# Kernel optimization log

Measured on AMD Instinct MI355X. Metric: run time of the kernel, lower is better.

Reference implementation:

```python
import jax, jax.numpy as jnp
import numpy as np

N_TEAMS = 100000
N_EDGES = 1600000
BATCH = 16384
DIM = 64
SLOPE = 0.01  # torch leaky_relu default


def setup_inputs() -> dict:
    key = jax.random.key(0)
    ks = jax.random.split(key, 12)
    return {
        "edge_index": jax.random.randint(ks[0], (2, N_EDGES), 0, N_TEAMS, dtype=jnp.int32),
        "edge_weight": jax.random.uniform(ks[1], (N_EDGES,), dtype=jnp.float32),
        "home": jax.random.randint(ks[2], (BATCH,), 0, N_TEAMS, dtype=jnp.int32),
        "away": jax.random.randint(ks[3], (BATCH,), 0, N_TEAMS, dtype=jnp.int32),
        "emb": jax.random.normal(ks[4], (N_TEAMS, DIM), dtype=jnp.float32),
        "W0": jax.random.normal(ks[5], (DIM, DIM), dtype=jnp.float32) * 0.1,
        "b0": jnp.zeros((DIM,), jnp.float32),
        "W1": jax.random.normal(ks[6], (DIM, DIM), dtype=jnp.float32) * 0.1,
        "b1": jnp.zeros((DIM,), jnp.float32),
        "W2": jax.random.normal(ks[7], (DIM, DIM), dtype=jnp.float32) * 0.1,
        "b2": jnp.zeros((DIM,), jnp.float32),
        "lin1_W": jax.random.normal(ks[8], (2 * DIM, 6), dtype=jnp.float32) * 0.1,
        "lin1_b": jnp.zeros((6,), jnp.float32),
        "lin3_W": jax.random.normal(ks[9], (6, 3), dtype=jnp.float32) * 0.1,
        "lin3_b": jnp.zeros((3,), jnp.float32),
    }


def gcn_conv(x, W, b, src, dst, w, n):
    """PyG GCNConv: add self-loops, symmetric edge-weight norm, gather-scale-scatter."""
    xw = x @ W  # [N, D_out]
    loop = jnp.arange(n, dtype=src.dtype)
    src2 = jnp.concatenate([src, loop])
    dst2 = jnp.concatenate([dst, loop])
    w2 = jnp.concatenate([w, jnp.ones((n,), x.dtype)])
    deg = jax.ops.segment_sum(w2, dst2, num_segments=n)
    dinv = jnp.where(deg > 0, jax.lax.rsqrt(jnp.maximum(deg, 1e-12)), 0.0)
    norm = dinv[src2] * w2 * dinv[dst2]  # [E+N]
    msgs = norm[:, None] * xw[src2]  # irregular gather, [E+N, D_out]
    return jax.ops.segment_sum(msgs, dst2, num_segments=n) + b


def reference(edge_index, edge_weight, home, away, emb, W0, b0, W1, b1, W2, b2,
              lin1_W, lin1_b, lin3_W, lin3_b):
    src, dst = edge_index[0], edge_index[1]
    n = emb.shape[0]
    x = emb  # embedding lookup of arange(n_teams) == full table
    x = jax.nn.leaky_relu(gcn_conv(x, W0, b0, src, dst, edge_weight, n), SLOPE)
    x = jax.nn.leaky_relu(gcn_conv(x, W1, b1, src, dst, edge_weight, n), SLOPE)
    x = jax.nn.leaky_relu(gcn_conv(x, W2, b2, src, dst, edge_weight, n), SLOPE)
    h = jnp.concatenate([x[home], x[away]], axis=-1)  # [B, 2*D]
    h = jax.nn.leaky_relu(h @ lin1_W + lin1_b, SLOPE)
    h = jax.nn.leaky_relu(h @ lin3_W + lin3_b, SLOPE)
    out = jax.nn.log_softmax(h, axis=0)  # original uses LogSoftmax(dim=0)
    return out.reshape(-1, 3)
```

## Files before the change

### kernel.cpp

```cpp
#include <hip/hip_runtime.h>
#include <hip/hip_fp8.h>
#include <math.h>

#define N_TEAMS 100000
#define N_EDGES 1600000
#define BATCH   16384
#define DIM     64
#define SLOPE   0.01f
#define NPAD    100352
#define BSHIFT  6
#define BROWS   64
#define NB      1563
#define SLOTS   8
#define SCAP    256

__device__ __forceinline__ float leaky(float v) { return v > 0.f ? v : SLOPE * v; }

__device__ __forceinline__ float bf2f(unsigned short u) {
    return __uint_as_float(((unsigned)u) << 16);
}
__device__ __forceinline__ unsigned short f2bf(float f) {
    unsigned b = __float_as_uint(f);
    unsigned r = b + 0x7FFFu + ((b >> 16) & 1u);
    return (unsigned short)(r >> 16);
}
__device__ __forceinline__ float f82f(unsigned char u) {
    __hip_fp8_e4m3 v; v.__x = (__hip_fp8_storage_t)u;
    return (float)v;
}
__device__ __forceinline__ unsigned char f2f8(float f) {
    __hip_fp8_e4m3 v(f);
    return (unsigned char)v.__x;
}
__device__ __forceinline__ float pw2f(unsigned p) {
    return __uint_as_float((p & 0xFFFE0000u) >> 1);
}


__global__ void k_zerob(int* __restrict__ bcnt) {
    int i = blockIdx.x * blockDim.x + threadIdx.x;
    if (i < NB * SLOTS) bcnt[i * 16] = 0;
}

__global__ void k_part(const int* __restrict__ src, const int* __restrict__ dst,
                       const float* __restrict__ w, int* __restrict__ bcnt,
                       unsigned long long* __restrict__ pbuf, int E) {
    int e = blockIdx.x * blockDim.x + threadIdx.x;
    if (e >= E) return;
    int slot = blockIdx.x & (SLOTS - 1);
    int s = __builtin_nontemporal_load(src + e);
    int d = __builtin_nontemporal_load(dst + e);
    float wv = __builtin_nontemporal_load(w + e);
    unsigned pk = (((unsigned)f2bf(wv) & 0x7FFFu) << 17) | (unsigned)s;
    int cell = (d >> BSHIFT) * SLOTS + slot;
    int p = atomicAdd(&bcnt[cell * 16], 1);
    pbuf[(size_t)cell * SCAP + p] = (((unsigned long long)d) << 32) | pk;
}

__global__ __launch_bounds__(256) void k_bcnt(const int* __restrict__ bcnt,
                                              const unsigned long long* __restrict__ pbuf,
                                              int* __restrict__ cnt) {
    __shared__ int h[BROWS];
    int b = blockIdx.x, tid = threadIdx.x;
    if (tid < BROWS) h[tid] = 0;
    __syncthreads();
    for (int slot = 0; slot < SLOTS; slot++) {
        int cell = b * SLOTS + slot;
        int n = bcnt[cell * 16];
        const unsigned long long* pb = pbuf + (size_t)cell * SCAP;
        for (int i = tid; i < n; i += 256) {
            int d = (int)(pb[i] >> 32);
            atomicAdd(&h[d & (BROWS - 1)], 1);
        }
    }
    __syncthreads();
    int row = b * BROWS + tid;
    if (tid < BROWS && row < NPAD) cnt[row] = h[tid];
}

__global__ __launch_bounds__(256) void k_scatter(const int* __restrict__ bcnt,
                                                 const unsigned long long* __restrict__ pbuf,
                                                 const int* __restrict__ row_start,
                                                 unsigned* __restrict__ edges) {
    __shared__ int fl[BROWS];
    int b = blockIdx.x, tid = threadIdx.x;
    if (tid < BROWS) fl[tid] = 0;
    __syncthreads();
    for (int slot = 0; slot < SLOTS; slot++) {
        int cell = b * SLOTS + slot;
        int n = bcnt[cell * 16];
        const unsigned long long* pb = pbuf + (size_t)cell * SCAP;
        for (int i = tid; i < n; i += 256) {
            unsigned long long rec = pb[i];
            int d = (int)(rec >> 32);
            int p = atomicAdd(&fl[d & (BROWS - 1)], 1);
            edges[row_start[d] + p] = (unsigned)rec;
        }
    }
}


__global__ __launch_bounds__(1024) void k_scan1(const int* __restrict__ cnt,
                                                int* __restrict__ excl,
                                                int* __restrict__ partial, int n) {
    __shared__ int s[1024];
    int tid = threadIdx.x;
    int i = blockIdx.x * 1024 + tid;
    int v = (i < n) ? cnt[i] : 0;
    s[tid] = v;
    __syncthreads();
    for (int off = 1; off < 1024; off <<= 1) {
        int t = (tid >= off) ? s[tid - off] : 0;
        __syncthreads();
        s[tid] += t;
        __syncthreads();
    }
    excl[i] = s[tid] - v;
    if (tid == 1023) partial[blockIdx.x] = s[1023];
}

__global__ __launch_bounds__(128) void k_scan2(int* __restrict__ partial, int nb) {
    __shared__ int s[128];
    int tid = threadIdx.x;
    int v = (tid < nb) ? partial[tid] : 0;
    s[tid] = v;
    __syncthreads();
    for (int off = 1; off < 128; off <<= 1) {
        int t = (tid >= off) ? s[tid - off] : 0;
        __syncthreads();
        s[tid] += t;
        __syncthreads();
    }
    if (tid < nb) partial[tid] = s[tid] - v;
}

__global__ __launch_bounds__(1024) void k_scan3(int* __restrict__ row_start,
                                                const int* __restrict__ partial) {
    int i = blockIdx.x * 1024 + threadIdx.x;
    row_start[i] += partial[blockIdx.x];
}


__global__ void k_dinv(const int* __restrict__ row_start,
                       const unsigned* __restrict__ edges,
                       float* __restrict__ dinv, int n) {
    int r = blockIdx.x * blockDim.x + threadIdx.x;
    if (r >= n) return;
    int beg = row_start[r], end = row_start[r + 1];
    float s = 1.0f;
    for (int j = beg; j < end; j++) s += pw2f(edges[j]);
    dinv[r] = rsqrtf(fmaxf(s, 1e-12f));
}


__global__ void k_cvt(const float* __restrict__ emb, unsigned short* __restrict__ y,
                      int n4) {
    int i = blockIdx.x * blockDim.x + threadIdx.x;
    if (i >= n4) return;
    float4 v = ((const float4*)emb)[i];
    ushort4 o;
    o.x = f2bf(v.x); o.y = f2bf(v.y); o.z = f2bf(v.z); o.w = f2bf(v.w);
    ((ushort4*)y)[i] = o;
}


__global__ __launch_bounds__(256) void k_gemm(
    const unsigned short* __restrict__ y, const float* __restrict__ W,
    const float* __restrict__ dinv, unsigned char* __restrict__ t8, int n) {
    __shared__ float Ws[64 * 64];
    __shared__ float xs[16 * 64];
    int tid = threadIdx.x;
    const float4* Wv = (const float4*)W;
    float4* Wsv = (float4*)Ws;
#pragma unroll
    for (int i = 0; i < 4; i++) Wsv[tid + i * 256] = Wv[tid + i * 256];
    int row0 = blockIdx.x * 16;
    {
        int idx = tid * 4;
        int r = idx >> 6, cc = idx & 63;
        ushort4 v = *(const ushort4*)(y + (((size_t)(row0 + r)) << 6) + cc);
        xs[idx + 0] = bf2f(v.x); xs[idx + 1] = bf2f(v.y);
        xs[idx + 2] = bf2f(v.z); xs[idx + 3] = bf2f(v.w);
    }
    __syncthreads();
    int c = tid & 63, rr = tid >> 6;
    float acc[4] = {0.f, 0.f, 0.f, 0.f};
#pragma unroll
    for (int k = 0; k < 64; k++) {
        float wv = Ws[k * 64 + c];
#pragma unroll
        for (int i = 0; i < 4; i++) acc[i] = fmaf(xs[(4 * i + rr) * 64 + k], wv, acc[i]);
    }
#pragma unroll
    for (int i = 0; i < 4; i++) {
        int r = row0 + 4 * i + rr;
        t8[(((size_t)r) << 6) + c] = f2f8(dinv[r] * acc[i]);
    }
}


__global__ __launch_bounds__(256) void k_agg(
    const unsigned char* __restrict__ t8, const int* __restrict__ row_start,
    const unsigned* __restrict__ edges, const float* __restrict__ dinv,
    const float* __restrict__ b, unsigned short* __restrict__ y, int n) {
    int tid = threadIdx.x;
    int lane = tid & 63;
    int row = blockIdx.x * 4 + (tid >> 6);
    if (row >= n) return;
    float bl = b[lane];
    int beg = row_start[row];
    int c = row_start[row + 1] - beg;
    float di = dinv[row];
    float acc = f82f(t8[((unsigned)row << 6) + lane]);
    const unsigned* ep = edges + beg;
    int j = 0;
    int chunks = c >> 3;
    if (chunks > 0) {
        unsigned ev[8];
#pragma unroll
        for (int k = 0; k < 8; k++) ev[k] = __builtin_nontemporal_load(ep + k);
        for (int t = 1; t <= chunks; t++) {
            float nv[8], xv[8];
#pragma unroll
            for (int k = 0; k < 8; k++) {
                int s = (int)(ev[k] & 0x1FFFFu);
                nv[k] = pw2f(ev[k]);
                xv[k] = f82f(t8[((unsigned)s << 6) + lane]);
            }
            if (t < chunks) {
                const unsigned* np = ep + (size_t)t * 8;
#pragma unroll
                for (int k = 0; k < 8; k++) ev[k] = __builtin_nontemporal_load(np + k);
            }
#pragma unroll
            for (int k = 0; k < 8; k++) acc = fmaf(nv[k], xv[k], acc);
        }
        j = chunks * 8;
    }
    if (j + 4 <= c) {
        unsigned e0 = __builtin_nontemporal_load(ep + j + 0);
        unsigned e1 = __builtin_nontemporal_load(ep + j + 1);
        unsigned e2 = __builtin_nontemporal_load(ep + j + 2);
        unsigned e3 = __builtin_nontemporal_load(ep + j + 3);
        float x0 = f82f(t8[((e0 & 0x1FFFFu) << 6) + lane]);
        float x1 = f82f(t8[((e1 & 0x1FFFFu) << 6) + lane]);
        float x2 = f82f(t8[((e2 & 0x1FFFFu) << 6) + lane]);
        float x3 = f82f(t8[((e3 & 0x1FFFFu) << 6) + lane]);
        acc = fmaf(pw2f(e0), x0, acc);
        acc = fmaf(pw2f(e1), x1, acc);
        acc = fmaf(pw2f(e2), x2, acc);
        acc = fmaf(pw2f(e3), x3, acc);
        j += 4;
    }
    for (; j < c; j++) {
        unsigned e0 = __builtin_nontemporal_load(ep + j);
        acc = fmaf(pw2f(e0), f82f(t8[((e0 & 0x1FFFFu) << 6) + lane]), acc);
    }
    y[((unsigned)row << 6) + lane] = f2bf(leaky(fmaf(di, acc, bl)));
}


__global__ __launch_bounds__(256) void k_head(
    const unsigned short* __restrict__ xb, const int* __restrict__ home,
    const int* __restrict__ away, const float* __restrict__ W1,
    const float* __restrict__ b1, const float* __restrict__ W3,
    const float* __restrict__ b3, float* __restrict__ z2, int B) {
    __shared__ float W1s[128 * 6];
    __shared__ float b1s[6], W3s[18], b3s[3];
    int tid = threadIdx.x;
    for (int i = tid; i < 768; i += 256) W1s[i] = W1[i];
    if (tid < 6) b1s[tid] = b1[tid];
    if (tid < 18) W3s[tid] = W3[tid];
    if (tid < 3) b3s[tid] = b3[tid];
    __syncthreads();
    int i = blockIdx.x * 256 + tid;
    if (i >= B) return;
    float z1[6];
#pragma unroll
    for (int j = 0; j < 6; j++) z1[j] = b1s[j];
    const uint4* rows[2];
    rows[0] = (const uint4*)(xb + (size_t)home[i] * 64);
    rows[1] = (const uint4*)(xb + (size_t)away[i] * 64);
#pragma unroll
    for (int h = 0; h < 2; h++) {
        const uint4* r = rows[h];
        int base = h * 64;
#pragma unroll
        for (int k = 0; k < 8; k++) {
            uint4 v = r[k];
            unsigned uu[4] = {v.x, v.y, v.z, v.w};
#pragma unroll
            for (int t = 0; t < 4; t++) {
                float fx = bf2f((unsigned short)(uu[t] & 0xFFFF));
                float fy = bf2f((unsigned short)(uu[t] >> 16));
                int d = base + k * 8 + t * 2;
#pragma unroll
                for (int j = 0; j < 6; j++) {
                    z1[j] = fmaf(fx, W1s[d * 6 + j], z1[j]);
                    z1[j] = fmaf(fy, W1s[(d + 1) * 6 + j], z1[j]);
                }
            }
        }
    }
#pragma unroll
    for (int j = 0; j < 6; j++) z1[j] = leaky(z1[j]);
#pragma unroll
    for (int c = 0; c < 3; c++) {
        float s = b3s[c];
#pragma unroll
        for (int j = 0; j < 6; j++) s = fmaf(z1[j], W3s[j * 3 + c], s);
        z2[(size_t)i * 3 + c] = leaky(s);
    }
}


__global__ __launch_bounds__(1024) void k_stats(const float* __restrict__ z2,
                                                float* __restrict__ stats, int B) {
    __shared__ float red[3][1024];
    int tid = threadIdx.x;
    float m[3] = {-1e30f, -1e30f, -1e30f};
    for (int i = tid; i < B; i += 1024) {
        m[0] = fmaxf(m[0], z2[3 * i + 0]);
        m[1] = fmaxf(m[1], z2[3 * i + 1]);
        m[2] = fmaxf(m[2], z2[3 * i + 2]);
    }
    for (int c = 0; c < 3; c++) red[c][tid] = m[c];
    __syncthreads();
    for (int s = 512; s > 0; s >>= 1) {
        if (tid < s)
            for (int c = 0; c < 3; c++) red[c][tid] = fmaxf(red[c][tid], red[c][tid + s]);
        __syncthreads();
    }
    float M[3];
    for (int c = 0; c < 3; c++) M[c] = red[c][0];
    __syncthreads();
    float sum[3] = {0.f, 0.f, 0.f};
    for (int i = tid; i < B; i += 1024) {
        sum[0] += expf(z2[3 * i + 0] - M[0]);
        sum[1] += expf(z2[3 * i + 1] - M[1]);
        sum[2] += expf(z2[3 * i + 2] - M[2]);
    }
    for (int c = 0; c < 3; c++) red[c][tid] = sum[c];
    __syncthreads();
    for (int s = 512; s > 0; s >>= 1) {
        if (tid < s)
            for (int c = 0; c < 3; c++) red[c][tid] += red[c][tid + s];
        __syncthreads();
    }
    if (tid == 0)
        for (int c = 0; c < 3; c++) { stats[c] = M[c]; stats[3 + c] = logf(red[c][0]); }
}

__global__ void k_final(const float* __restrict__ z2, const float* __restrict__ stats,
                        float* __restrict__ out, int n) {
    int i = blockIdx.x * blockDim.x + threadIdx.x;
    if (i < n) {
        int c = i % 3;
        out[i] = z2[i] - stats[c] - stats[3 + c];
    }
}


extern "C" void kernel_launch(void* const* d_in, const int* in_sizes, int n_in,
                              void* d_out, int out_size, void* d_ws, size_t ws_size,
                              hipStream_t stream) {
    const int*   edge_index = (const int*)d_in[0];
    const int*   src  = edge_index;
    const int*   dst  = edge_index + N_EDGES;
    const float* ew   = (const float*)d_in[1];
    const int*   home = (const int*)d_in[2];
    const int*   away = (const int*)d_in[3];
    const float* emb  = (const float*)d_in[4];
    const float* W0 = (const float*)d_in[5];  const float* b0 = (const float*)d_in[6];
    const float* W1 = (const float*)d_in[7];  const float* b1 = (const float*)d_in[8];
    const float* W2 = (const float*)d_in[9];  const float* b2 = (const float*)d_in[10];
    const float* l1W = (const float*)d_in[11]; const float* l1b = (const float*)d_in[12];
    const float* l3W = (const float*)d_in[13]; const float* l3b = (const float*)d_in[14];

    char* p = (char*)d_ws;
    float*              dinv      = (float*)p;              p += NPAD * 4;
    int*                cnt       = (int*)p;                p += NPAD * 4;
    int*                row_start = (int*)p;                p += (NPAD + 1024) * 4;
    int*                partial   = (int*)p;                p += 128 * 4;
    int*                bcnt      = (int*)p;                p += (size_t)NB * SLOTS * 16 * 4;
    unsigned*           edges     = (unsigned*)p;           p += (size_t)N_EDGES * 4;
    unsigned char*      t8        = (unsigned char*)p;      p += (size_t)N_TEAMS * 64;
    unsigned short*     Y         = (unsigned short*)p;     p += (size_t)N_TEAMS * 64 * 2;
    unsigned long long* pbuf      = (unsigned long long*)p; p += (size_t)NB * SLOTS * SCAP * 8;
    float*              z2        = (float*)p;              p += (size_t)BATCH * 3 * 4;
    float*              stats     = (float*)p;

    const int scanBlocks = NPAD / 1024;

    k_zerob<<<(NB * SLOTS + 255) / 256, 256, 0, stream>>>(bcnt);
    k_part<<<(N_EDGES + 255) / 256, 256, 0, stream>>>(src, dst, ew, bcnt, pbuf, N_EDGES);
    k_bcnt<<<NB, 256, 0, stream>>>(bcnt, pbuf, cnt);
    k_scan1<<<scanBlocks, 1024, 0, stream>>>(cnt, row_start, partial, N_TEAMS);
    k_scan2<<<1, 128, 0, stream>>>(partial, scanBlocks);
    k_scan3<<<scanBlocks, 1024, 0, stream>>>(row_start, partial);
    k_scatter<<<NB, 256, 0, stream>>>(bcnt, pbuf, row_start, edges);
    k_dinv<<<(N_TEAMS + 255) / 256, 256, 0, stream>>>(row_start, edges, dinv, N_TEAMS);
    k_cvt<<<(N_TEAMS * 16 + 255) / 256, 256, 0, stream>>>(emb, Y, N_TEAMS * 16);

    const int GBLOCKS = N_TEAMS / 16;
    const int ABLOCKS = (N_TEAMS + 3) / 4;

    k_gemm<<<GBLOCKS, 256, 0, stream>>>(Y, W0, dinv, t8, N_TEAMS);
    k_agg<<<ABLOCKS, 256, 0, stream>>>(t8, row_start, edges, dinv, b0, Y, N_TEAMS);
    k_gemm<<<GBLOCKS, 256, 0, stream>>>(Y, W1, dinv, t8, N_TEAMS);
    k_agg<<<ABLOCKS, 256, 0, stream>>>(t8, row_start, edges, dinv, b1, Y, N_TEAMS);
    k_gemm<<<GBLOCKS, 256, 0, stream>>>(Y, W2, dinv, t8, N_TEAMS);
    k_agg<<<ABLOCKS, 256, 0, stream>>>(t8, row_start, edges, dinv, b2, Y, N_TEAMS);

    k_head<<<(BATCH + 255) / 256, 256, 0, stream>>>(Y, home, away, l1W, l1b, l3W, l3b, z2, BATCH);
    k_stats<<<1, 1024, 0, stream>>>(z2, stats, BATCH);
    k_final<<<(BATCH * 3 + 255) / 256, 256, 0, stream>>>(z2, stats, (float*)d_out, BATCH * 3);
}
```

Baseline: 409.7 us.

## Pick partition slot by XCC id and fuse degree computation into bucket count

The edge-partition kernel now chooses its slot from the hardware XCC id instead of the block index, so blocks on one XCC share a slot's counters. This keeps atomic contention and writes local to each die's L2. Slot capacity is raised and writes beyond it are dropped. The separate dinv kernel is removed; degree sums are accumulated with shared-memory float atomics in k_bcnt, saving a pass over the CSR edges. The risk is that records past SCAP are silently lost if the split across XCCs is uneven, and float atomics make the degree sum order nondeterministic.

```diff
diff --git a/kernel.cpp b/kernel.cpp
--- a/kernel.cpp
+++ b/kernel.cpp
@@ -12,9 +12,15 @@
 #define BROWS   64
 #define NB      1563
 #define SLOTS   8
-#define SCAP    256
+#define SCAP    384
 
 __device__ __forceinline__ float leaky(float v) { return v > 0.f ? v : SLOPE * v; }
+
+__device__ __forceinline__ int xcc_id() {
+    int x;
+    asm volatile("s_getreg_b32 %0, hwreg(HW_REG_XCC_ID)" : "=s"(x));
+    return x & (SLOTS - 1);
+}
 
 __device__ __forceinline__ float bf2f(unsigned short u) {
     return __uint_as_float(((unsigned)u) << 16);
@@ -47,35 +53,42 @@
                        unsigned long long* __restrict__ pbuf, int E) {
     int e = blockIdx.x * blockDim.x + threadIdx.x;
     if (e >= E) return;
-    int slot = blockIdx.x & (SLOTS - 1);
+    int slot = xcc_id();
     int s = __builtin_nontemporal_load(src + e);
     int d = __builtin_nontemporal_load(dst + e);
     float wv = __builtin_nontemporal_load(w + e);
     unsigned pk = (((unsigned)f2bf(wv) & 0x7FFFu) << 17) | (unsigned)s;
     int cell = (d >> BSHIFT) * SLOTS + slot;
     int p = atomicAdd(&bcnt[cell * 16], 1);
-    pbuf[(size_t)cell * SCAP + p] = (((unsigned long long)d) << 32) | pk;
+    if (p < SCAP) pbuf[(size_t)cell * SCAP + p] = (((unsigned long long)d) << 32) | pk;
 }
 
 __global__ __launch_bounds__(256) void k_bcnt(const int* __restrict__ bcnt,
                                               const unsigned long long* __restrict__ pbuf,
-                                              int* __restrict__ cnt) {
+                                              int* __restrict__ cnt,
+                                              float* __restrict__ dinv) {
     __shared__ int h[BROWS];
+    __shared__ float ws[BROWS];
     int b = blockIdx.x, tid = threadIdx.x;
-    if (tid < BROWS) h[tid] = 0;
+    if (tid < BROWS) { h[tid] = 0; ws[tid] = 0.f; }
     __syncthreads();
     for (int slot = 0; slot < SLOTS; slot++) {
         int cell = b * SLOTS + slot;
         int n = bcnt[cell * 16];
         const unsigned long long* pb = pbuf + (size_t)cell * SCAP;
         for (int i = tid; i < n; i += 256) {
-            int d = (int)(pb[i] >> 32);
+            unsigned long long rec = pb[i];
+            int d = (int)(rec >> 32);
             atomicAdd(&h[d & (BROWS - 1)], 1);
+            atomicAdd(&ws[d & (BROWS - 1)], pw2f((unsigned)rec));
         }
     }
     __syncthreads();
     int row = b * BROWS + tid;
-    if (tid < BROWS && row < NPAD) cnt[row] = h[tid];
+    if (tid < BROWS && row < NPAD) {
+        cnt[row] = h[tid];
+        dinv[row] = rsqrtf(fmaxf(1.0f + ws[tid], 1e-12f));
+    }
 }
 
 __global__ __launch_bounds__(256) void k_scatter(const int* __restrict__ bcnt,
@@ -138,18 +151,6 @@
                                                 const int* __restrict__ partial) {
     int i = blockIdx.x * 1024 + threadIdx.x;
     row_start[i] += partial[blockIdx.x];
-}
-
-
-__global__ void k_dinv(const int* __restrict__ row_start,
-                       const unsigned* __restrict__ edges,
-                       float* __restrict__ dinv, int n) {
-    int r = blockIdx.x * blockDim.x + threadIdx.x;
-    if (r >= n) return;
-    int beg = row_start[r], end = row_start[r + 1];
-    float s = 1.0f;
-    for (int j = beg; j < end; j++) s += pw2f(edges[j]);
-    dinv[r] = rsqrtf(fmaxf(s, 1e-12f));
 }
 
 
@@ -394,12 +395,11 @@
 
     k_zerob<<<(NB * SLOTS + 255) / 256, 256, 0, stream>>>(bcnt);
     k_part<<<(N_EDGES + 255) / 256, 256, 0, stream>>>(src, dst, ew, bcnt, pbuf, N_EDGES);
-    k_bcnt<<<NB, 256, 0, stream>>>(bcnt, pbuf, cnt);
+    k_bcnt<<<NB, 256, 0, stream>>>(bcnt, pbuf, cnt, dinv);
     k_scan1<<<scanBlocks, 1024, 0, stream>>>(cnt, row_start, partial, N_TEAMS);
     k_scan2<<<1, 128, 0, stream>>>(partial, scanBlocks);
     k_scan3<<<scanBlocks, 1024, 0, stream>>>(row_start, partial);
     k_scatter<<<NB, 256, 0, stream>>>(bcnt, pbuf, row_start, edges);
-    k_dinv<<<(N_TEAMS + 255) / 256, 256, 0, stream>>>(row_start, edges, dinv, N_TEAMS);
     k_cvt<<<(N_TEAMS * 16 + 255) / 256, 256, 0, stream>>>(emb, Y, N_TEAMS * 16);
 
     const int GBLOCKS = N_TEAMS / 16;
```

Measured after the change: 412.0 us. No clear change (+0.5%).
